# Kernel optimization log

Hardware: AMD Instinct MI355X
Metric: run time of the kernel (lower is better)

Reference implementation:

```python
import jax, jax.numpy as jnp
import numpy as np

N = 50000          # num nodes
E = 800000         # num edges (avg degree 16)
R = 8              # num relations
IN = 128
H0 = 256
H1 = 64


def _w(key, shape, fan_in):
    return jax.random.normal(key, shape, dtype=jnp.float32) * (1.0 / np.sqrt(fan_in))


def setup_inputs() -> dict:
    key = jax.random.key(0)
    ks = jax.random.split(key, 16)
    x = jax.random.normal(ks[0], (N, IN), dtype=jnp.float32)
    edge_index = jax.random.randint(ks[1], (2, E), 0, N, dtype=jnp.int64)
    edge_type = jax.random.randint(ks[2], (E,), 0, R, dtype=jnp.int64)
    return {
        "x": x,
        "edge_index": edge_index,
        "edge_type": edge_type,
        # RGCNConv params: per-relation weights [R, in, out], root weight [in, out], bias [out]
        "W1": _w(ks[3], (R, IN, H0), IN), "root1": _w(ks[4], (IN, H0), IN), "b1": jnp.zeros((H0,), jnp.float32),
        "W2": _w(ks[5], (R, H0, H0), H0), "root2": _w(ks[6], (H0, H0), H0), "b2": jnp.zeros((H0,), jnp.float32),
        "W3": _w(ks[7], (R, H0, H0), H0), "root3": _w(ks[8], (H0, H0), H0), "b3": jnp.zeros((H0,), jnp.float32),
        "W4": _w(ks[9], (R, H0, H1), H0), "root4": _w(ks[10], (H0, H1), H0), "b4": jnp.zeros((H1,), jnp.float32),
    }


def rgcn_layer(x, edge_index, edge_type, W, root, bias):
    """PyG RGCNConv: out_i = x_i @ root + sum_r (1/|N_r(i)|) sum_{j in N_r(i)} x_j @ W_r + bias.
    Aggregation is linear, so aggregate source features per (relation, dst) first,
    then apply the R small GEMMs — avoids per-edge [E, out] message materialization."""
    src, dst = edge_index[0], edge_index[1]
    seg = edge_type * N + dst                      # combined (relation, dst) segment id
    nseg = R * N
    agg = jax.ops.segment_sum(x[src], seg, num_segments=nseg)          # [R*N, in]
    cnt = jax.ops.segment_sum(jnp.ones((seg.shape[0],), x.dtype), seg, num_segments=nseg)
    agg = agg / jnp.maximum(cnt, 1.0)[:, None]                          # mean per (r, i)
    agg = agg.reshape(R, N, x.shape[1])                                 # [R, N, in]
    return jnp.einsum('rni,rio->no', agg, W) + x @ root + bias


def reference(x, edge_index, edge_type, W1, root1, b1, W2, root2, b2, W3, root3, b3, W4, root4, b4):
    h = jax.nn.relu(rgcn_layer(x, edge_index, edge_type, W1, root1, b1))
    h = jax.nn.relu(rgcn_layer(h, edge_index, edge_type, W2, root2, b2))
    h = jax.nn.relu(rgcn_layer(h, edge_index, edge_type, W3, root3, b3))
    return rgcn_layer(h, edge_index, edge_type, W4, root4, b4)
```

## Files before the change

kernel.cpp:

```cpp
#include <hip/hip_runtime.h>

#define N_NODES 50000
#define N_PAD   50048
#define N_EDGES 800000
#define N_REL   8
#define NSEG    (N_REL * N_NODES)
#define SCAN_NB 391

typedef short bf16x8 __attribute__((ext_vector_type(8)));
typedef float f32x4  __attribute__((ext_vector_type(4)));

__device__ __forceinline__ ushort f2bf(float f) {
    union { float f; unsigned u; } c; c.f = f;
    unsigned u = c.u + 0x7fffu + ((c.u >> 16) & 1u);
    return (ushort)(u >> 16);
}
__device__ __forceinline__ void add8(float* s, uint4 v) {
    unsigned u[4] = {v.x, v.y, v.z, v.w};
    #pragma unroll
    for (int k = 0; k < 4; ++k) {
        s[2 * k]     += __uint_as_float(u[k] << 16);
        s[2 * k + 1] += __uint_as_float(u[k] & 0xffff0000u);
    }
}
__device__ __forceinline__ void async16(const ushort* g, ushort* l) {
    __builtin_amdgcn_global_load_lds((const __attribute__((address_space(1))) void*)g,
                                     (__attribute__((address_space(3))) void*)l, 16, 0, 0);
}


__global__ void count_edges(const int* __restrict__ dst, const int* __restrict__ et,
                            int* __restrict__ cnt) {
    int e = blockIdx.x * 256 + threadIdx.x;
    if (e < N_EDGES) atomicAdd(&cnt[et[e] * N_NODES + dst[e]], 1);
}

__global__ __launch_bounds__(256) void scan_pass1(const int* __restrict__ cnt,
                                                  int* __restrict__ sums) {
    __shared__ int sc[256];
    int b = blockIdx.x, t = threadIdx.x;
    int base = b * 1024 + t * 4;
    int v = 0;
    #pragma unroll
    for (int i = 0; i < 4; ++i) { int idx = base + i; if (idx < NSEG) v += cnt[idx]; }
    sc[t] = v; __syncthreads();
    for (int off = 1; off < 256; off <<= 1) {
        int x = (t >= off) ? sc[t - off] : 0;
        __syncthreads(); sc[t] += x; __syncthreads();
    }
    if (t == 255) sums[b] = sc[255];
}

__global__ __launch_bounds__(512) void scan_pass2(int* __restrict__ sums, int nb) {
    __shared__ int sc[512];
    int t = threadIdx.x;
    int v = (t < nb) ? sums[t] : 0;
    sc[t] = v; __syncthreads();
    for (int off = 1; off < 512; off <<= 1) {
        int x = (t >= off) ? sc[t - off] : 0;
        __syncthreads(); sc[t] += x; __syncthreads();
    }
    if (t < nb) sums[t] = sc[t] - v;
}

__global__ __launch_bounds__(256) void scan_pass3(const int* __restrict__ cnt,
                                                  const int* __restrict__ sums,
                                                  int* __restrict__ row_ptr) {
    __shared__ int sc[256];
    int b = blockIdx.x, t = threadIdx.x;
    int base = b * 1024 + t * 4;
    int e[4]; int v = 0;
    #pragma unroll
    for (int i = 0; i < 4; ++i) { int idx = base + i; e[i] = (idx < NSEG) ? cnt[idx] : 0; v += e[i]; }
    sc[t] = v; __syncthreads();
    for (int off = 1; off < 256; off <<= 1) {
        int x = (t >= off) ? sc[t - off] : 0;
        __syncthreads(); sc[t] += x; __syncthreads();
    }
    int run = sums[b] + (sc[t] - v);
    #pragma unroll
    for (int i = 0; i < 4; ++i) {
        int idx = base + i;
        if (idx < NSEG) row_ptr[idx] = run;
        run += e[i];
    }
    if (b == 0 && t == 0) row_ptr[NSEG] = N_EDGES;
}

__global__ void place_edges(const int* __restrict__ src, const int* __restrict__ dst,
                            const int* __restrict__ et, const int* __restrict__ row_ptr,
                            int* __restrict__ cnt, int* __restrict__ sorted_src) {
    int e = blockIdx.x * 256 + threadIdx.x;
    if (e >= N_EDGES) return;
    int key = et[e] * N_NODES + dst[e];
    int old = atomicSub(&cnt[key], 1);
    sorted_src[row_ptr[key] + old - 1] = src[e];
}


__global__ void convert_weights(const float* __restrict__ W, const float* __restrict__ root,
                                ushort* __restrict__ BT, int K, int O, int NPAD) {
    int idx = blockIdx.x * 256 + threadIdx.x;
    if (idx >= NPAD * K) return;
    int col = idx / K, i = idx % K;
    float v = 0.0f;
    if (col < N_REL * O) {
        int r = col / O, o = col % O;
        v = W[((size_t)r * K + i) * O + o];
    } else if (col < (N_REL + 1) * O) {
        v = root[(size_t)i * O + (col - N_REL * O)];
    }
    BT[idx] = f2bf(v);
}

__global__ void f32_to_bf16(const float* __restrict__ in, ushort* __restrict__ out, int n4) {
    int i = blockIdx.x * 256 + threadIdx.x;
    if (i >= n4) return;
    float4 v = ((const float4*)in)[i];
    ushort4 s; s.x = f2bf(v.x); s.y = f2bf(v.y); s.z = f2bf(v.z); s.w = f2bf(v.w);
    ((ushort4*)out)[i] = s;
}

template<int K>
__global__ __launch_bounds__(256)
void gemm_mfma(const ushort* __restrict__ A, const ushort* __restrict__ BT,
               ushort* __restrict__ Y, int NW) {
    __shared__ ushort SMEM[9216];
    ushort* As = SMEM;
    ushort* Bs = SMEM + 4096;
    const int t = threadIdx.x;
    const int lane = t & 63;
    const int w = t >> 6;
    const int l16 = lane & 15, q = lane >> 4;
    const int wm = (w & 1) * 64, wn = (w >> 1) * 64;
    const int col0 = blockIdx.x * 128;
    const int row0 = blockIdx.y * 128;

    const int c0i = w * 64 + lane;
    const int c1i = c0i + 256;
    const size_t ga0 = (size_t)(c0i >> 2) * K + (size_t)(c0i & 3) * 8;
    const size_t ga1 = (size_t)(c1i >> 2) * K + (size_t)(c1i & 3) * 8;
    const ushort* Ab = A + (size_t)row0 * K;
    const ushort* Bb = BT + (size_t)col0 * K;
    ushort* lA0 = &As[w * 512];
    ushort* lA1 = &As[(w + 4) * 512];
    ushort* lB0 = &Bs[w * 512];
    ushort* lB1 = &Bs[(w + 4) * 512];

    f32x4 acc[4][4] = {};

    #pragma unroll
    for (int k0 = 0; k0 < K; k0 += 32) {
        __syncthreads();
        async16(Ab + k0 + ga0, lA0);
        async16(Ab + k0 + ga1, lA1);
        async16(Bb + k0 + ga0, lB0);
        async16(Bb + k0 + ga1, lB1);
        __syncthreads();
        bf16x8 a[4], b[4];
        #pragma unroll
        for (int i = 0; i < 4; ++i) {
            a[i] = *(const bf16x8*)&As[(wm + i * 16 + l16) * 32 + q * 8];
            b[i] = *(const bf16x8*)&Bs[(wn + i * 16 + l16) * 32 + q * 8];
        }
        #pragma unroll
        for (int i = 0; i < 4; ++i)
            #pragma unroll
            for (int j = 0; j < 4; ++j)
                acc[i][j] = __builtin_amdgcn_mfma_f32_16x16x32_bf16(a[i], b[j], acc[i][j], 0, 0, 0);
    }

    __syncthreads();
    ushort* Ts = &SMEM[w * 32 * 72];
    const int rr = lane >> 3;
    const int cc = (lane & 7) * 8;
    #pragma unroll
    for (int half = 0; half < 2; ++half) {
        #pragma unroll
        for (int i = 0; i < 2; ++i)
            #pragma unroll
            for (int j = 0; j < 4; ++j)
                #pragma unroll
                for (int r = 0; r < 4; ++r)
                    Ts[(i * 16 + q * 4 + r) * 72 + j * 16 + l16] = f2bf(acc[half * 2 + i][j][r]);
        #pragma unroll
        for (int p = 0; p < 4; ++p) {
            int row = p * 8 + rr;
            uint4 v = *(const uint4*)&Ts[row * 72 + cc];
            *(uint4*)(Y + (size_t)(row0 + wm + half * 32 + row) * NW + col0 + wn + cc) = v;
        }
    }
}

template<int O>
__global__ __launch_bounds__(256)
void gather_kernel(const ushort* __restrict__ Y, int NW,
                   const int* __restrict__ row_ptr, const int* __restrict__ sorted_src,
                   const float* __restrict__ bias,
                   float* __restrict__ out_f32, ushort* __restrict__ out_bf16, int relu) {
    constexpr int TPN = O / 8;
    int d = blockIdx.x * (256 / TPN) + threadIdx.x / TPN;
    if (d >= N_NODES) return;
    int c0 = (threadIdx.x % TPN) * 8;
    float sum[8] = {};
    add8(sum, *(const uint4*)(Y + (size_t)d * NW + N_REL * O + c0));
    #pragma unroll
    for (int k = 0; k < 8; ++k) sum[k] += bias[c0 + k];
    for (int r = 0; r < N_REL; ++r) {
        int base = r * N_NODES + d;
        int s0 = row_ptr[base], s1 = row_ptr[base + 1];
        if (s1 <= s0) continue;
        float ps[8] = {};
        const ushort* Yc = Y + r * O + c0;
        for (int e = s0; e < s1; ++e)
            add8(ps, *(const uint4*)(Yc + (size_t)sorted_src[e] * NW));
        float inv = 1.0f / (float)(s1 - s0);
        #pragma unroll
        for (int k = 0; k < 8; ++k) sum[k] += ps[k] * inv;
    }
    if (relu) {
        #pragma unroll
        for (int k = 0; k < 8; ++k) sum[k] = fmaxf(sum[k], 0.0f);
    }
    if (out_bf16) {
        ushort o[8];
        #pragma unroll
        for (int k = 0; k < 8; ++k) o[k] = f2bf(sum[k]);
        *(uint4*)(out_bf16 + (size_t)d * O + c0) = *(const uint4*)o;
    } else {
        float* p = out_f32 + (size_t)d * O + c0;
        *(float4*)p = make_float4(sum[0], sum[1], sum[2], sum[3]);
        *(float4*)(p + 4) = make_float4(sum[4], sum[5], sum[6], sum[7]);
    }
}


extern "C" void kernel_launch(void* const* d_in, const int* in_sizes, int n_in,
                              void* d_out, int out_size, void* d_ws, size_t ws_size,
                              hipStream_t stream) {
    const float* x  = (const float*)d_in[0];
    const int*   ei = (const int*)d_in[1];
    const int*   et = (const int*)d_in[2];
    const float* W[4]  = {(const float*)d_in[3], (const float*)d_in[6], (const float*)d_in[9],  (const float*)d_in[12]};
    const float* RT[4] = {(const float*)d_in[4], (const float*)d_in[7], (const float*)d_in[10], (const float*)d_in[13]};
    const float* BI[4] = {(const float*)d_in[5], (const float*)d_in[8], (const float*)d_in[11], (const float*)d_in[14]};
    const int KS[4] = {128, 256, 256, 256};
    const int OS[4] = {256, 256, 256, 64};
    const int NP[4] = {2304, 2304, 2304, 640};
    const int* src = ei;
    const int* dst = ei + N_EDGES;

    char* ws = (char*)d_ws;
    size_t off = 0;
    auto take = [&](size_t bytes) -> char* {
        char* p = ws + off;
        off = (off + bytes + 255) & ~(size_t)255;
        return p;
    };
    int* cnt        = (int*)take((size_t)NSEG * 4);
    int* row_ptr    = (int*)take((size_t)(NSEG + 1) * 4);
    int* sums       = (int*)take(512 * 4);
    int* sorted_src = (int*)take((size_t)N_EDGES * 4);
    ushort* BTp[4];
    for (int l = 0; l < 4; ++l) BTp[l] = (ushort*)take((size_t)NP[l] * KS[l] * 2);
    ushort* hb = (ushort*)take((size_t)N_PAD * 256 * 2);
    ushort* Yb = (ushort*)take((size_t)N_PAD * 2304 * 2);

    hipMemsetAsync(cnt, 0, (size_t)NSEG * 4, stream);
    count_edges<<<(N_EDGES + 255) / 256, 256, 0, stream>>>(dst, et, cnt);
    scan_pass1<<<SCAN_NB, 256, 0, stream>>>(cnt, sums);
    scan_pass2<<<1, 512, 0, stream>>>(sums, SCAN_NB);
    scan_pass3<<<SCAN_NB, 256, 0, stream>>>(cnt, sums, row_ptr);
    place_edges<<<(N_EDGES + 255) / 256, 256, 0, stream>>>(src, dst, et, row_ptr, cnt, sorted_src);

    for (int l = 0; l < 4; ++l) {
        int n = NP[l] * KS[l];
        convert_weights<<<(n + 255) / 256, 256, 0, stream>>>(W[l], RT[l], BTp[l], KS[l], OS[l], NP[l]);
    }

    f32_to_bf16<<<(N_NODES * 128 / 4 + 255) / 256, 256, 0, stream>>>(x, hb, N_NODES * 128 / 4);

    for (int l = 0; l < 4; ++l) {
        const int K = KS[l], O = OS[l];
        dim3 g(NP[l] / 128, N_PAD / 128), b(256);
        if (K == 128) gemm_mfma<128><<<g, b, 0, stream>>>(hb, BTp[l], Yb, NP[l]);
        else          gemm_mfma<256><<<g, b, 0, stream>>>(hb, BTp[l], Yb, NP[l]);
        if (O == 256)
            gather_kernel<256><<<dim3((N_NODES + 7) / 8), 256, 0, stream>>>(
                Yb, NP[l], row_ptr, sorted_src, BI[l], nullptr, hb, 1);
        else
            gather_kernel<64><<<dim3((N_NODES + 31) / 32), 256, 0, stream>>>(
                Yb, NP[l], row_ptr, sorted_src, BI[l], (float*)d_out, nullptr, 0);
    }
}
```

Measured before the change: 765.8 us.

## Aggregate neighbor features before GEMM and fuse bias/ReLU into concatenated-K GEMM

Layers 1-3 now do the per-relation mean aggregation on the narrow input features h. The results go into a concatenated [N, 9K] buffer that also holds the root term. A new GEMM then multiplies it by stacked [W_r; root] weights, applying bias and ReLU in its epilogue. This replaces the old order of transform-then-gather, where each edge did a random read from a wide 2304-column GEMM output. Random reads now hit the small h table, which should fit in cache. The cost is a large Agg buffer that is written and read again, and a GEMM with a long K dimension and single-stage register prefetch. The last layer keeps the transform-then-gather path.

```diff
diff --git a/kernel.cpp b/kernel.cpp
--- a/kernel.cpp
+++ b/kernel.cpp
@@ -98,8 +98,20 @@
 }
 
 
-__global__ void convert_weights(const float* __restrict__ W, const float* __restrict__ root,
-                                ushort* __restrict__ BT, int K, int O, int NPAD) {
+__global__ void convert_cat(const float* __restrict__ W, const float* __restrict__ root,
+                            ushort* __restrict__ BT, int K) {
+    int KT = 9 * K;
+    int idx = blockIdx.x * 256 + threadIdx.x;
+    if (idx >= 256 * KT) return;
+    int col = idx / KT, kk = idx % KT;
+    int r = kk / K, i = kk % K;
+    float v = (r < N_REL) ? W[((size_t)r * K + i) * 256 + col] : root[(size_t)i * 256 + col];
+    BT[idx] = f2bf(v);
+}
+
+__global__ void convert_t4(const float* __restrict__ W, const float* __restrict__ root,
+                           ushort* __restrict__ BT) {
+    const int K = 256, O = 64, NPAD = 640;
     int idx = blockIdx.x * 256 + threadIdx.x;
     if (idx >= NPAD * K) return;
     int col = idx / K, i = idx % K;
@@ -119,6 +131,109 @@
     float4 v = ((const float4*)in)[i];
     ushort4 s; s.x = f2bf(v.x); s.y = f2bf(v.y); s.z = f2bf(v.z); s.w = f2bf(v.w);
     ((ushort4*)out)[i] = s;
+}
+
+template<int K>
+__global__ __launch_bounds__(256)
+void segsum_kernel(const ushort* __restrict__ h, const int* __restrict__ row_ptr,
+                   const int* __restrict__ sorted_src, ushort* __restrict__ Agg) {
+    constexpr int TPN = K / 8;
+    constexpr int DPB = 256 / TPN;
+    constexpr int KT = 9 * K;
+    int d = blockIdx.x * DPB + (int)threadIdx.x / TPN;
+    int r = blockIdx.y;
+    int c0 = ((int)threadIdx.x % TPN) * 8;
+    if (d >= N_PAD) return;
+    ushort* outp = Agg + (size_t)d * KT + r * K + c0;
+    if (d >= N_NODES) { *(uint4*)outp = make_uint4(0u, 0u, 0u, 0u); return; }
+    if (r == N_REL) {
+        *(uint4*)outp = *(const uint4*)(h + (size_t)d * K + c0);
+        return;
+    }
+    int base = r * N_NODES + d;
+    int s0 = row_ptr[base], s1 = row_ptr[base + 1];
+    float sum[8] = {};
+    for (int e = s0; e < s1; ++e)
+        add8(sum, *(const uint4*)(h + (size_t)sorted_src[e] * K + c0));
+    float inv = (s1 > s0) ? 1.0f / (float)(s1 - s0) : 0.0f;
+    ushort o[8];
+    #pragma unroll
+    for (int k = 0; k < 8; ++k) o[k] = f2bf(sum[k] * inv);
+    *(uint4*)outp = *(const uint4*)o;
+}
+
+template<int KT>
+__global__ __launch_bounds__(256)
+void gemm_ag(const ushort* __restrict__ A, const ushort* __restrict__ BT,
+             const float* __restrict__ bias, ushort* __restrict__ Out) {
+    __shared__ ushort SMEM[10240];
+    ushort* As = SMEM;
+    ushort* Bs = SMEM + 2048;
+    const int t = threadIdx.x;
+    const int lane = t & 63, w = t >> 6;
+    const int l16 = lane & 15, q = lane >> 4;
+    const int wn = w * 64;
+    const int row0 = blockIdx.x * 64;
+
+    const ushort* Aptr = A + (size_t)(row0 + (t >> 2)) * KT + ((t & 3) << 3);
+    const ushort* Bptr = BT + (size_t)(t >> 2) * KT + ((t & 3) << 3);
+
+    uint4 rA = *(const uint4*)Aptr;
+    uint4 rB[4];
+    #pragma unroll
+    for (int p = 0; p < 4; ++p) rB[p] = *(const uint4*)(Bptr + (size_t)p * 64 * KT);
+
+    f32x4 acc[4][4] = {};
+
+    for (int k0 = 0; k0 < KT; k0 += 32) {
+        __syncthreads();
+        *(uint4*)&As[t * 8] = rA;
+        #pragma unroll
+        for (int p = 0; p < 4; ++p) *(uint4*)&Bs[(p * 256 + t) * 8] = rB[p];
+        if (k0 + 32 < KT) {
+            rA = *(const uint4*)(Aptr + k0 + 32);
+            #pragma unroll
+            for (int p = 0; p < 4; ++p)
+                rB[p] = *(const uint4*)(Bptr + (size_t)p * 64 * KT + k0 + 32);
+        }
+        __syncthreads();
+        bf16x8 a[4], b[4];
+        #pragma unroll
+        for (int i = 0; i < 4; ++i) {
+            a[i] = *(const bf16x8*)&As[(i * 16 + l16) * 32 + q * 8];
+            b[i] = *(const bf16x8*)&Bs[(wn + i * 16 + l16) * 32 + q * 8];
+        }
+        #pragma unroll
+        for (int i = 0; i < 4; ++i)
+            #pragma unroll
+            for (int j = 0; j < 4; ++j)
+                acc[i][j] = __builtin_amdgcn_mfma_f32_16x16x32_bf16(a[i], b[j], acc[i][j], 0, 0, 0);
+    }
+
+    __syncthreads();
+    ushort* Ts = &SMEM[w * 2304];
+    const int rr = lane >> 3;
+    const int cc = (lane & 7) * 8;
+    #pragma unroll
+    for (int half = 0; half < 2; ++half) {
+        #pragma unroll
+        for (int i = 0; i < 2; ++i)
+            #pragma unroll
+            for (int j = 0; j < 4; ++j) {
+                float bv = bias[wn + j * 16 + l16];
+                #pragma unroll
+                for (int r = 0; r < 4; ++r) {
+                    float v = fmaxf(acc[half * 2 + i][j][r] + bv, 0.0f);
+                    Ts[(i * 16 + q * 4 + r) * 72 + j * 16 + l16] = f2bf(v);
+                }
+            }
+        #pragma unroll
+        for (int p = 0; p < 4; ++p) {
+            int row = p * 8 + rr;
+            uint4 v = *(const uint4*)&Ts[row * 72 + cc];
+            *(uint4*)(Out + (size_t)(row0 + half * 32 + row) * 256 + wn + cc) = v;
+        }
+    }
 }
 
 template<int K>
@@ -192,18 +307,16 @@
     }
 }
 
-template<int O>
 __global__ __launch_bounds__(256)
-void gather_kernel(const ushort* __restrict__ Y, int NW,
-                   const int* __restrict__ row_ptr, const int* __restrict__ sorted_src,
-                   const float* __restrict__ bias,
-                   float* __restrict__ out_f32, ushort* __restrict__ out_bf16, int relu) {
-    constexpr int TPN = O / 8;
-    int d = blockIdx.x * (256 / TPN) + threadIdx.x / TPN;
+void gather64(const ushort* __restrict__ Y, int NW,
+              const int* __restrict__ row_ptr, const int* __restrict__ sorted_src,
+              const float* __restrict__ bias, float* __restrict__ out) {
+    constexpr int TPN = 8;
+    int d = blockIdx.x * 32 + threadIdx.x / TPN;
     if (d >= N_NODES) return;
     int c0 = (threadIdx.x % TPN) * 8;
     float sum[8] = {};
-    add8(sum, *(const uint4*)(Y + (size_t)d * NW + N_REL * O + c0));
+    add8(sum, *(const uint4*)(Y + (size_t)d * NW + N_REL * 64 + c0));
     #pragma unroll
     for (int k = 0; k < 8; ++k) sum[k] += bias[c0 + k];
     for (int r = 0; r < N_REL; ++r) {
@@ -211,27 +324,16 @@
         int s0 = row_ptr[base], s1 = row_ptr[base + 1];
         if (s1 <= s0) continue;
         float ps[8] = {};
-        const ushort* Yc = Y + r * O + c0;
+        const ushort* Yc = Y + r * 64 + c0;
         for (int e = s0; e < s1; ++e)
             add8(ps, *(const uint4*)(Yc + (size_t)sorted_src[e] * NW));
         float inv = 1.0f / (float)(s1 - s0);
         #pragma unroll
         for (int k = 0; k < 8; ++k) sum[k] += ps[k] * inv;
     }
-    if (relu) {
-        #pragma unroll
-        for (int k = 0; k < 8; ++k) sum[k] = fmaxf(sum[k], 0.0f);
-    }
-    if (out_bf16) {
-        ushort o[8];
-        #pragma unroll
-        for (int k = 0; k < 8; ++k) o[k] = f2bf(sum[k]);
-        *(uint4*)(out_bf16 + (size_t)d * O + c0) = *(const uint4*)o;
-    } else {
-        float* p = out_f32 + (size_t)d * O + c0;
-        *(float4*)p = make_float4(sum[0], sum[1], sum[2], sum[3]);
-        *(float4*)(p + 4) = make_float4(sum[4], sum[5], sum[6], sum[7]);
-    }
+    float* p = out + (size_t)d * 64 + c0;
+    *(float4*)p = make_float4(sum[0], sum[1], sum[2], sum[3]);
+    *(float4*)(p + 4) = make_float4(sum[4], sum[5], sum[6], sum[7]);
 }
 
 
@@ -244,9 +346,6 @@
     const float* W[4]  = {(const float*)d_in[3], (const float*)d_in[6], (const float*)d_in[9],  (const float*)d_in[12]};
     const float* RT[4] = {(const float*)d_in[4], (const float*)d_in[7], (const float*)d_in[10], (const float*)d_in[13]};
     const float* BI[4] = {(const float*)d_in[5], (const float*)d_in[8], (const float*)d_in[11], (const float*)d_in[14]};
-    const int KS[4] = {128, 256, 256, 256};
-    const int OS[4] = {256, 256, 256, 64};
-    const int NP[4] = {2304, 2304, 2304, 640};
     const int* src = ei;
     const int* dst = ei + N_EDGES;
 
@@ -261,10 +360,12 @@
     int* row_ptr    = (int*)take((size_t)(NSEG + 1) * 4);
     int* sums       = (int*)take(512 * 4);
     int* sorted_src = (int*)take((size_t)N_EDGES * 4);
-    ushort* BTp[4];
-    for (int l = 0; l < 4; ++l) BTp[l] = (ushort*)take((size_t)NP[l] * KS[l] * 2);
-    ushort* hb = (ushort*)take((size_t)N_PAD * 256 * 2);
-    ushort* Yb = (ushort*)take((size_t)N_PAD * 2304 * 2);
+    ushort* BTc0 = (ushort*)take((size_t)256 * 1152 * 2);
+    ushort* BTc1 = (ushort*)take((size_t)256 * 2304 * 2);
+    ushort* BTc2 = (ushort*)take((size_t)256 * 2304 * 2);
+    ushort* BT4  = (ushort*)take((size_t)640 * 256 * 2);
+    ushort* hb   = (ushort*)take((size_t)N_PAD * 256 * 2);
+    ushort* Agg  = (ushort*)take((size_t)N_PAD * 2304 * 2);
 
     hipMemsetAsync(cnt, 0, (size_t)NSEG * 4, stream);
     count_edges<<<(N_EDGES + 255) / 256, 256, 0, stream>>>(dst, et, cnt);
@@ -273,23 +374,23 @@
     scan_pass3<<<SCAN_NB, 256, 0, stream>>>(cnt, sums, row_ptr);
     place_edges<<<(N_EDGES + 255) / 256, 256, 0, stream>>>(src, dst, et, row_ptr, cnt, sorted_src);
 
-    for (int l = 0; l < 4; ++l) {
-        int n = NP[l] * KS[l];
-        convert_weights<<<(n + 255) / 256, 256, 0, stream>>>(W[l], RT[l], BTp[l], KS[l], OS[l], NP[l]);
-    }
+    convert_cat<<<(256 * 1152 + 255) / 256, 256, 0, stream>>>(W[0], RT[0], BTc0, 128);
+    convert_cat<<<(256 * 2304 + 255) / 256, 256, 0, stream>>>(W[1], RT[1], BTc1, 256);
+    convert_cat<<<(256 * 2304 + 255) / 256, 256, 0, stream>>>(W[2], RT[2], BTc2, 256);
+    convert_t4<<<(640 * 256 + 255) / 256, 256, 0, stream>>>(W[3], RT[3], BT4);
 
     f32_to_bf16<<<(N_NODES * 128 / 4 + 255) / 256, 256, 0, stream>>>(x, hb, N_NODES * 128 / 4);
 
-    for (int l = 0; l < 4; ++l) {
-        const int K = KS[l], O = OS[l];
-        dim3 g(NP[l] / 128, N_PAD / 128), b(256);
-        if (K == 128) gemm_mfma<128><<<g, b, 0, stream>>>(hb, BTp[l], Yb, NP[l]);
-        else          gemm_mfma<256><<<g, b, 0, stream>>>(hb, BTp[l], Yb, NP[l]);
-        if (O == 256)
-            gather_kernel<256><<<dim3((N_NODES + 7) / 8), 256, 0, stream>>>(
-                Yb, NP[l], row_ptr, sorted_src, BI[l], nullptr, hb, 1);
-        else
-            gather_kernel<64><<<dim3((N_NODES + 31) / 32), 256, 0, stream>>>(
-                Yb, NP[l], row_ptr, sorted_src, BI[l], (float*)d_out, nullptr, 0);
-    }
-}
+    segsum_kernel<128><<<dim3(N_PAD / 16, 9), 256, 0, stream>>>(hb, row_ptr, sorted_src, Agg);
+    gemm_ag<1152><<<N_PAD / 64, 256, 0, stream>>>(Agg, BTc0, BI[0], hb);
+
+    segsum_kernel<256><<<dim3(N_PAD / 8, 9), 256, 0, stream>>>(hb, row_ptr, sorted_src, Agg);
+    gemm_ag<2304><<<N_PAD / 64, 256, 0, stream>>>(Agg, BTc1, BI[1], hb);
+
+    segsum_kernel<256><<<dim3(N_PAD / 8, 9), 256, 0, stream>>>(hb, row_ptr, sorted_src, Agg);
+    gemm_ag<2304><<<N_PAD / 64, 256, 0, stream>>>(Agg, BTc2, BI[2], hb);
+
+    dim3 g4(640 / 128, N_PAD / 128);
+    gemm_mfma<256><<<g4, 256, 0, stream>>>(hb, BT4, Agg, 640);
+    gather64<<<(N_NODES + 31) / 32, 256, 0, stream>>>(Agg, 640, row_ptr, sorted_src, BI[3], (float*)d_out);
+}
```

Result: slower. 1.408 ms (+83.9%).

## Restructure GEMM to keep A row-stripe resident in LDS and sweep all column tiles

Applied to the files above, without the earlier changes.

Replaces the 2D-tiled MFMA GEMM with a stripe kernel. Each block loads a 64-row slice of the activations into shared memory once, then loops over every 128-column tile of the weight matrix, double-buffering B tiles with async loads and writing each finished tile out. This avoids reloading A for every column tile and overlaps B loads with compute, at the cost of fewer, longer-running blocks (782) and more shared memory per block. The gather kernel now loads all row_ptr bounds up front, and the padded rows of the bf16 activation buffer are zeroed.

```diff
diff --git a/kernel.cpp b/kernel.cpp
--- a/kernel.cpp
+++ b/kernel.cpp
@@ -121,73 +121,83 @@
     ((ushort4*)out)[i] = s;
 }
 
-template<int K>
+template<int K, int CTS, int OUTW>
 __global__ __launch_bounds__(256)
-void gemm_mfma(const ushort* __restrict__ A, const ushort* __restrict__ BT,
-               ushort* __restrict__ Y, int NW) {
-    __shared__ ushort SMEM[9216];
-    ushort* As = SMEM;
-    ushort* Bs = SMEM + 4096;
+void gemm_stripe(const ushort* __restrict__ A, const ushort* __restrict__ BT,
+                 ushort* __restrict__ Y) {
+    constexpr int AP  = K + 8;
+    constexpr int KST = K / 32;
+    constexpr int NS  = CTS * KST;
+    __shared__ ushort As[64 * AP];
+    __shared__ ushort Bs[2][4096];
+    __shared__ ushort Ts[4 * 1152];
     const int t = threadIdx.x;
-    const int lane = t & 63;
-    const int w = t >> 6;
+    const int lane = t & 63, w = t >> 6;
     const int l16 = lane & 15, q = lane >> 4;
-    const int wm = (w & 1) * 64, wn = (w >> 1) * 64;
-    const int col0 = blockIdx.x * 128;
-    const int row0 = blockIdx.y * 128;
-
-    const int c0i = w * 64 + lane;
-    const int c1i = c0i + 256;
-    const size_t ga0 = (size_t)(c0i >> 2) * K + (size_t)(c0i & 3) * 8;
-    const size_t ga1 = (size_t)(c1i >> 2) * K + (size_t)(c1i & 3) * 8;
-    const ushort* Ab = A + (size_t)row0 * K;
-    const ushort* Bb = BT + (size_t)col0 * K;
-    ushort* lA0 = &As[w * 512];
-    ushort* lA1 = &As[(w + 4) * 512];
-    ushort* lB0 = &Bs[w * 512];
-    ushort* lB1 = &Bs[(w + 4) * 512];
-
-    f32x4 acc[4][4] = {};
-
-    #pragma unroll
-    for (int k0 = 0; k0 < K; k0 += 32) {
+    const int wm = (w & 1) * 32, wn = (w >> 1) * 64;
+    const int row0 = blockIdx.x * 64;
+
+    {
+        constexpr int RC = K / 8;
+        #pragma unroll
+        for (int i = 0; i < 64 * RC / 256; ++i) {
+            int c = i * 256 + t;
+            int row = c / RC, ko = (c % RC) * 8;
+            uint4 v = *(const uint4*)(A + (size_t)(row0 + row) * K + ko);
+            *(uint4*)&As[row * AP + ko] = v;
+        }
+    }
+
+    const int cB = w * 64 + lane;
+    const int bcol = cB >> 2, bko = (cB & 3) * 8;
+    auto stageB = [&](int s, int buf) {
+        const ushort* Bb = BT + (size_t)((s / KST) * 128) * K + (s % KST) * 32;
+        async16(Bb + (size_t)bcol * K + bko, &Bs[buf][cB * 8]);
+        async16(Bb + (size_t)(bcol + 64) * K + bko, &Bs[buf][cB * 8 + 2048]);
+    };
+
+    f32x4 acc[2][4] = {};
+    stageB(0, 0);
+
+    for (int s = 0; s < NS; ++s) {
+        const int buf = s & 1;
         __syncthreads();
-        async16(Ab + k0 + ga0, lA0);
-        async16(Ab + k0 + ga1, lA1);
-        async16(Bb + k0 + ga0, lB0);
-        async16(Bb + k0 + ga1, lB1);
-        __syncthreads();
-        bf16x8 a[4], b[4];
-        #pragma unroll
-        for (int i = 0; i < 4; ++i) {
-            a[i] = *(const bf16x8*)&As[(wm + i * 16 + l16) * 32 + q * 8];
-            b[i] = *(const bf16x8*)&Bs[(wn + i * 16 + l16) * 32 + q * 8];
-        }
-        #pragma unroll
-        for (int i = 0; i < 4; ++i)
+        if (s + 1 < NS) stageB(s + 1, buf ^ 1);
+        const int k0 = (s % KST) * 32;
+        bf16x8 a[2], b[4];
+        #pragma unroll
+        for (int i = 0; i < 2; ++i)
+            a[i] = *(const bf16x8*)&As[(wm + i * 16 + l16) * AP + k0 + q * 8];
+        #pragma unroll
+        for (int j = 0; j < 4; ++j)
+            b[j] = *(const bf16x8*)&Bs[buf][(wn + j * 16 + l16) * 32 + q * 8];
+        #pragma unroll
+        for (int i = 0; i < 2; ++i)
             #pragma unroll
             for (int j = 0; j < 4; ++j)
                 acc[i][j] = __builtin_amdgcn_mfma_f32_16x16x32_bf16(a[i], b[j], acc[i][j], 0, 0, 0);
-    }
-
-    __syncthreads();
-    ushort* Ts = &SMEM[w * 32 * 72];
-    const int rr = lane >> 3;
-    const int cc = (lane & 7) * 8;
-    #pragma unroll
-    for (int half = 0; half < 2; ++half) {
-        #pragma unroll
-        for (int i = 0; i < 2; ++i)
+
+        if ((s + 1) % KST == 0) {
+            const int ct = s / KST;
+            ushort* Tw = &Ts[w * 1152];
+            const int rr = lane >> 3, cc = (lane & 7) * 8;
             #pragma unroll
-            for (int j = 0; j < 4; ++j)
+            for (int i = 0; i < 2; ++i) {
                 #pragma unroll
-                for (int r = 0; r < 4; ++r)
-                    Ts[(i * 16 + q * 4 + r) * 72 + j * 16 + l16] = f2bf(acc[half * 2 + i][j][r]);
-        #pragma unroll
-        for (int p = 0; p < 4; ++p) {
-            int row = p * 8 + rr;
-            uint4 v = *(const uint4*)&Ts[row * 72 + cc];
-            *(uint4*)(Y + (size_t)(row0 + wm + half * 32 + row) * NW + col0 + wn + cc) = v;
+                for (int j = 0; j < 4; ++j)
+                    #pragma unroll
+                    for (int r = 0; r < 4; ++r)
+                        Tw[(q * 4 + r) * 72 + j * 16 + l16] = f2bf(acc[i][j][r]);
+                #pragma unroll
+                for (int p = 0; p < 2; ++p) {
+                    int row = p * 8 + rr;
+                    uint4 v = *(const uint4*)&Tw[row * 72 + cc];
+                    *(uint4*)(Y + (size_t)(row0 + wm + i * 16 + row) * OUTW
+                              + ct * 128 + wn + cc) = v;
+                }
+                #pragma unroll
+                for (int j = 0; j < 4; ++j) acc[i][j] = (f32x4){0.f, 0.f, 0.f, 0.f};
+            }
         }
     }
 }
@@ -202,19 +212,23 @@
     int d = blockIdx.x * (256 / TPN) + threadIdx.x / TPN;
     if (d >= N_NODES) return;
     int c0 = (threadIdx.x % TPN) * 8;
+    int s0[N_REL], s1[N_REL];
+    #pragma unroll
+    for (int r = 0; r < N_REL; ++r) {
+        s0[r] = row_ptr[r * N_NODES + d];
+        s1[r] = row_ptr[r * N_NODES + d + 1];
+    }
     float sum[8] = {};
     add8(sum, *(const uint4*)(Y + (size_t)d * NW + N_REL * O + c0));
     #pragma unroll
     for (int k = 0; k < 8; ++k) sum[k] += bias[c0 + k];
     for (int r = 0; r < N_REL; ++r) {
-        int base = r * N_NODES + d;
-        int s0 = row_ptr[base], s1 = row_ptr[base + 1];
-        if (s1 <= s0) continue;
+        if (s1[r] <= s0[r]) continue;
         float ps[8] = {};
         const ushort* Yc = Y + r * O + c0;
-        for (int e = s0; e < s1; ++e)
+        for (int e = s0[r]; e < s1[r]; ++e)
             add8(ps, *(const uint4*)(Yc + (size_t)sorted_src[e] * NW));
-        float inv = 1.0f / (float)(s1 - s0);
+        float inv = 1.0f / (float)(s1[r] - s0[r]);
         #pragma unroll
         for (int k = 0; k < 8; ++k) sum[k] += ps[k] * inv;
     }
@@ -279,17 +293,21 @@
     }
 
     f32_to_bf16<<<(N_NODES * 128 / 4 + 255) / 256, 256, 0, stream>>>(x, hb, N_NODES * 128 / 4);
-
-    for (int l = 0; l < 4; ++l) {
-        const int K = KS[l], O = OS[l];
-        dim3 g(NP[l] / 128, N_PAD / 128), b(256);
-        if (K == 128) gemm_mfma<128><<<g, b, 0, stream>>>(hb, BTp[l], Yb, NP[l]);
-        else          gemm_mfma<256><<<g, b, 0, stream>>>(hb, BTp[l], Yb, NP[l]);
-        if (O == 256)
-            gather_kernel<256><<<dim3((N_NODES + 7) / 8), 256, 0, stream>>>(
-                Yb, NP[l], row_ptr, sorted_src, BI[l], nullptr, hb, 1);
-        else
-            gather_kernel<64><<<dim3((N_NODES + 31) / 32), 256, 0, stream>>>(
-                Yb, NP[l], row_ptr, sorted_src, BI[l], (float*)d_out, nullptr, 0);
-    }
-}
+    hipMemsetAsync(hb + (size_t)N_NODES * 128, 0, (size_t)(N_PAD - N_NODES) * 128 * 2, stream);
+
+    gemm_stripe<128, 18, 2304><<<N_PAD / 64, 256, 0, stream>>>(hb, BTp[0], Yb);
+    gather_kernel<256><<<dim3((N_NODES + 7) / 8), 256, 0, stream>>>(
+        Yb, 2304, row_ptr, sorted_src, BI[0], nullptr, hb, 1);
+
+    gemm_stripe<256, 18, 2304><<<N_PAD / 64, 256, 0, stream>>>(hb, BTp[1], Yb);
+    gather_kernel<256><<<dim3((N_NODES + 7) / 8), 256, 0, stream>>>(
+        Yb, 2304, row_ptr, sorted_src, BI[1], nullptr, hb, 1);
+
+    gemm_stripe<256, 18, 2304><<<N_PAD / 64, 256, 0, stream>>>(hb, BTp[2], Yb);
+    gather_kernel<256><<<dim3((N_NODES + 7) / 8), 256, 0, stream>>>(
+        Yb, 2304, row_ptr, sorted_src, BI[2], nullptr, hb, 1);
+
+    gemm_stripe<256, 5, 640><<<N_PAD / 64, 256, 0, stream>>>(hb, BTp[3], Yb);
+    gather_kernel<64><<<dim3((N_NODES + 31) / 32), 256, 0, stream>>>(
+        Yb, 640, row_ptr, sorted_src, BI[3], (float*)d_out, nullptr, 0);
+}
```

Result: slower. 970.0 us (+26.7%).
